# Optimization experiments

Measured on AMD Instinct MI355X. Metric: run time of the kernel, lower is better.

The kernel has to match this reference:

```python
import math
import jax, jax.numpy as jnp
import numpy as np

H_HEADS = 8
K_MAX = 64
MIN_WINDOW = 1.0
SHARPNESS = 5.0


def rmsnorm(x, w, eps=1e-6):
    x32 = x.astype(jnp.float32)
    var = jnp.mean(x32 * x32, axis=-1, keepdims=True)
    return (w * (x32 * jax.lax.rsqrt(var + eps))).astype(x.dtype)


def setup_inputs() -> dict:
    key = jax.random.key(0)
    ks = jax.random.split(key, 12)
    B, L, C = 1, 4096, 256
    H, K = H_HEADS, K_MAX
    s = 0.02
    return {
        "x": jax.random.normal(ks[0], (B, L, C), jnp.float32),
        "window_w": jax.random.normal(ks[1], (C, H), jnp.float32) * s,
        "window_b": jnp.zeros((H,), jnp.float32),
        "window_gamma": jnp.ones((H,), jnp.float32),
        "offset_w": jax.random.normal(ks[2], (C, H), jnp.float32) * s,
        "offset_b": jnp.zeros((H,), jnp.float32),
        "offset_gamma": jnp.ones((H,), jnp.float32),
        "kernel_w": jax.random.normal(ks[3], (C, H * K), jnp.float32) * s,
        "kernel_b": jnp.zeros((H * K,), jnp.float32),
        "kernel_gamma": jnp.ones((H * K,), jnp.float32),
        "v_w": jax.random.normal(ks[4], (C, C), jnp.float32) * (1.0 / math.sqrt(C)),
        "v_b": jnp.zeros((C,), jnp.float32),
        "out_w": jax.random.normal(ks[5], (C, C), jnp.float32) * s,
    }


def reference(x, window_w, window_b, window_gamma, offset_w, offset_b, offset_gamma,
              kernel_w, kernel_b, kernel_gamma, v_w, v_b, out_w):
    B, L, C = x.shape
    H, K = H_HEADS, K_MAX
    D = C // H
    max_window = min(int(math.sqrt(L)), K)
    half = max_window // 2
    max_offset = int(math.sqrt(L))
    N = 2 * half + 1  # num_offsets

    # per-position learned window sizes, center offsets, kernel weights
    window_raw = jax.nn.sigmoid(rmsnorm(x @ window_w + window_b, window_gamma))
    window_sizes = MIN_WINDOW + window_raw * (max_window - MIN_WINDOW)      # [B,L,H]
    center_offsets = jnp.tanh(rmsnorm(x @ offset_w + offset_b, offset_gamma)) * max_offset  # [B,L,H]
    kernel_weights = jax.nn.silu(rmsnorm(x @ kernel_w + kernel_b, kernel_gamma)).reshape(B, L, H, K)
    v = (x @ v_w + v_b).reshape(B, L, H, D)

    local = jnp.arange(-half, half + 1, dtype=x.dtype)                      # [N]
    positions = jnp.arange(L, dtype=x.dtype).reshape(1, L, 1, 1)
    neighbor = positions + center_offsets[..., None] + local.reshape(1, 1, 1, N)  # [B,L,H,N]
    valid = (neighbor >= 0) & (neighbor < L)
    nclamp = jnp.clip(neighbor, 0, L - 1)

    rel = jnp.abs(local).reshape(1, 1, 1, N) / (window_sizes[..., None] / 2 + 1e-6)
    window_mask = jax.nn.sigmoid(SHARPNESS * (1.0 - rel)) * valid.astype(x.dtype)

    # kernel interpolation by relative distance
    kidx = jnp.clip(rel, 0, 1) * (K - 1)
    i_fl = jnp.clip(kidx.astype(jnp.int32), 0, K - 2)                       # [B,L,H,N]
    i_ce = i_fl + 1
    w_ce = kidx - i_fl.astype(x.dtype)
    k_fl = jnp.take_along_axis(kernel_weights, i_fl, axis=-1)
    k_ce = jnp.take_along_axis(kernel_weights, i_ce, axis=-1)
    kernel_interp = k_fl * (1.0 - w_ce) + k_ce * w_ce

    attn = kernel_interp * window_mask
    attn = attn / (jnp.sum(attn, axis=-1, keepdims=True) + 1e-6)            # [B,L,H,N]

    # bilinear gather of values at fractional neighbor positions
    p_fl = jnp.clip(jnp.floor(nclamp).astype(jnp.int32), 0, L - 1)
    p_ce = jnp.clip(p_fl + 1, 0, L - 1)
    frac = nclamp - p_fl.astype(x.dtype)                                    # [B,L,H,N]

    v_bh = v.transpose(0, 2, 1, 3)                                          # [B,H,L,D]
    idx_f = p_fl.transpose(0, 2, 1, 3).reshape(B, H, L * N)
    idx_c = p_ce.transpose(0, 2, 1, 3).reshape(B, H, L * N)
    v_fl = jnp.take_along_axis(v_bh, idx_f[..., None], axis=2).reshape(B, H, L, N, D)
    v_ce = jnp.take_along_axis(v_bh, idx_c[..., None], axis=2).reshape(B, H, L, N, D)
    frac_bh = frac.transpose(0, 2, 1, 3)[..., None]                         # [B,H,L,N,1]
    v_nb = v_fl * (1.0 - frac_bh) + v_ce * frac_bh                          # [B,H,L,N,D]

    attn_bh = attn.transpose(0, 2, 1, 3)                                    # [B,H,L,N]
    out = jnp.einsum('bhln,bhlnd->bhld', attn_bh, v_nb)                     # [B,H,L,D]
    out = out.transpose(0, 2, 1, 3).reshape(B, L, C)
    return jax.nn.silu(out @ out_w)
```

## Files before the change

### kernel.cpp

```cpp
#include <hip/hip_runtime.h>
#include <math.h>

#define L_SEQ 4096
#define C_DIM 256
#define H_HEADS 8
#define K_MAX 64
#define D_HEAD 32
#define HALF_W 32
#define N_OFF 65
#define HK 512

__device__ __forceinline__ float sigmoidf_(float x) { return 1.0f / (1.0f + expf(-x)); }

__global__ void proj_gemm(const float* __restrict__ A, const float* __restrict__ kw_w,
                          const float* __restrict__ vw, const float* __restrict__ kb,
                          const float* __restrict__ vb,
                          float* __restrict__ kwbuf, float* __restrict__ vbuf) {
    __shared__ float As[16][132];
    __shared__ float Bs[16][68];

    const int tid = threadIdx.x;
    const int tx = tid & 15;
    const int ty = tid >> 4;
    const int l0 = blockIdx.y * 128;
    const int n0 = blockIdx.x * 64;

    const int ar0 = tid >> 2;
    const int ac0 = (tid & 3) * 4;
    const int ar1 = ar0 + 64;
    const int bk = tid >> 4;
    const int bn = (tid & 15) * 4;

    const float* Bsrc;
    int ldb, coff;
    if (n0 < 512) { Bsrc = kw_w; ldb = 512; coff = n0; }
    else          { Bsrc = vw;   ldb = 256; coff = n0 - 512; }

    float acc[8][4];
#pragma unroll
    for (int i = 0; i < 8; ++i)
#pragma unroll
        for (int jj = 0; jj < 4; ++jj) acc[i][jj] = 0.0f;

    float4 av0 = *(const float4*)&A[(l0 + ar0) * C_DIM + ac0];
    float4 av1 = *(const float4*)&A[(l0 + ar1) * C_DIM + ac0];
    float4 bv  = *(const float4*)&Bsrc[bk * ldb + coff + bn];

    for (int k0 = 0; k0 < C_DIM; k0 += 16) {
        __syncthreads();
        As[ac0 + 0][ar0] = av0.x;
        As[ac0 + 1][ar0] = av0.y;
        As[ac0 + 2][ar0] = av0.z;
        As[ac0 + 3][ar0] = av0.w;
        As[ac0 + 0][ar1] = av1.x;
        As[ac0 + 1][ar1] = av1.y;
        As[ac0 + 2][ar1] = av1.z;
        As[ac0 + 3][ar1] = av1.w;
        *(float4*)&Bs[bk][bn] = bv;
        __syncthreads();
        if (k0 + 16 < C_DIM) {
            av0 = *(const float4*)&A[(l0 + ar0) * C_DIM + (k0 + 16) + ac0];
            av1 = *(const float4*)&A[(l0 + ar1) * C_DIM + (k0 + 16) + ac0];
            bv  = *(const float4*)&Bsrc[(k0 + 16 + bk) * ldb + coff + bn];
        }
#pragma unroll
        for (int kk = 0; kk < 16; ++kk) {
            const float4 a4lo = *(const float4*)&As[kk][ty * 8];
            const float4 a4hi = *(const float4*)&As[kk][ty * 8 + 4];
            const float4 b4   = *(const float4*)&Bs[kk][tx * 4];
            const float ar[8] = {a4lo.x, a4lo.y, a4lo.z, a4lo.w,
                                 a4hi.x, a4hi.y, a4hi.z, a4hi.w};
            const float br[4] = {b4.x, b4.y, b4.z, b4.w};
#pragma unroll
            for (int i = 0; i < 8; ++i)
#pragma unroll
                for (int jj = 0; jj < 4; ++jj)
                    acc[i][jj] = fmaf(ar[i], br[jj], acc[i][jj]);
        }
    }

    const int g0 = n0 + tx * 4;
    float4 bz;
    float* dst;
    int stride, col;
    if (g0 < 512) { bz = *(const float4*)&kb[g0];       dst = kwbuf; stride = 512; col = g0; }
    else          { bz = *(const float4*)&vb[g0 - 512]; dst = vbuf;  stride = 256; col = g0 - 512; }
#pragma unroll
    for (int i = 0; i < 8; ++i) {
        const int row = l0 + ty * 8 + i;
        float4 o;
        o.x = acc[i][0] + bz.x;
        o.y = acc[i][1] + bz.y;
        o.z = acc[i][2] + bz.z;
        o.w = acc[i][3] + bz.w;
        *(float4*)&dst[row * stride + col] = o;
    }
}

__global__ void conv_fused(const float* __restrict__ x,
                           const float* __restrict__ ww, const float* __restrict__ wb,
                           const float* __restrict__ wg,
                           const float* __restrict__ ow, const float* __restrict__ ob,
                           const float* __restrict__ og,
                           const float* __restrict__ kg,
                           const float* __restrict__ kwraw, const float* __restrict__ v,
                           float* __restrict__ out) {
    const int l = blockIdx.x;
    const int tid = threadIdx.x;

    __shared__ float red[256];
    __shared__ float rs_s;
    __shared__ float kwrow[HK];
    __shared__ float wsz[H_HEADS], ofs[H_HEADS];
    __shared__ float4 tap[H_HEADS][N_OFF];
    __shared__ float inv_denom[H_HEADS];

    {
        const int j = tid;
        const float* row = kwraw + l * HK;
        const float z0 = row[j];
        const float z1 = row[j + 256];
        red[j] = z0 * z0 + z1 * z1;
        __syncthreads();
        for (int s = 128; s > 0; s >>= 1) {
            if (j < s) red[j] += red[j + s];
            __syncthreads();
        }
        if (j == 0) rs_s = rsqrtf(red[0] / (float)HK + 1e-6f);
        __syncthreads();
        const float rs = rs_s;
        const float n0v = kg[j] * z0 * rs;
        const float n1v = kg[j + 256] * z1 * rs;
        kwrow[j]       = n0v * sigmoidf_(n0v);
        kwrow[j + 256] = n1v * sigmoidf_(n1v);
    }

    if (tid < 64) {
        const int lane = tid;
        const float* xr = x + l * C_DIM;
        float accw[H_HEADS], acco[H_HEADS];
#pragma unroll
        for (int h = 0; h < H_HEADS; ++h) { accw[h] = 0.0f; acco[h] = 0.0f; }
#pragma unroll
        for (int i = 0; i < C_DIM / 64; ++i) {
            const int c = lane + i * 64;
            const float xv = xr[c];
            const float* wwc = ww + c * H_HEADS;
            const float* owc = ow + c * H_HEADS;
#pragma unroll
            for (int h = 0; h < H_HEADS; ++h) {
                accw[h] = fmaf(xv, wwc[h], accw[h]);
                acco[h] = fmaf(xv, owc[h], acco[h]);
            }
        }
#pragma unroll
        for (int off = 32; off > 0; off >>= 1) {
#pragma unroll
            for (int h = 0; h < H_HEADS; ++h) {
                accw[h] += __shfl_xor(accw[h], off);
                acco[h] += __shfl_xor(acco[h], off);
            }
        }
        if (lane < H_HEADS) {
            float zw[H_HEADS], zo[H_HEADS];
            float ssw = 0.0f, sso = 0.0f;
#pragma unroll
            for (int h = 0; h < H_HEADS; ++h) {
                zw[h] = accw[h] + wb[h];
                zo[h] = acco[h] + ob[h];
                ssw += zw[h] * zw[h];
                sso += zo[h] * zo[h];
            }
            const float rw = rsqrtf(ssw / (float)H_HEADS + 1e-6f);
            const float ro = rsqrtf(sso / (float)H_HEADS + 1e-6f);
            const float nw = wg[lane] * zw[lane] * rw;
            const float no = og[lane] * zo[lane] * ro;
            wsz[lane] = 1.0f + sigmoidf_(nw) * 63.0f;
            ofs[lane] = tanhf(no) * 64.0f;
        }
    }
    __syncthreads();

    for (int t = tid; t < H_HEADS * N_OFF; t += 256) {
        const int h = t / N_OFF;
        const int n = t - h * N_OFF;
        const float ws  = wsz[h];
        const float off = ofs[h];
        const float local = (float)(n - HALF_W);
        const float neighbor = (float)l + off + local;
        const bool valid = (neighbor >= 0.0f) && (neighbor < (float)L_SEQ);
        const float nc = fminf(fmaxf(neighbor, 0.0f), (float)(L_SEQ - 1));

        const float rel = fabsf(local) / (ws * 0.5f + 1e-6f);
        const float mask = sigmoidf_(5.0f * (1.0f - rel)) * (valid ? 1.0f : 0.0f);

        const float kidx = fminf(rel, 1.0f) * (float)(K_MAX - 1);
        int ifl = (int)kidx;
        ifl = min(ifl, K_MAX - 2);
        const float wce = kidx - (float)ifl;
        const float kf = kwrow[h * K_MAX + ifl];
        const float kc = kwrow[h * K_MAX + ifl + 1];
        const float attnv = (kf * (1.0f - wce) + kc * wce) * mask;

        int p = (int)floorf(nc);
        p = min(max(p, 0), L_SEQ - 1);
        const int pc = min(p + 1, L_SEQ - 1);
        const float fr = nc - (float)p;

        float4 tv;
        tv.x = attnv;
        tv.y = fr;
        tv.z = __int_as_float(p * C_DIM + h * D_HEAD);
        tv.w = __int_as_float(pc * C_DIM + h * D_HEAD);
        tap[h][n] = tv;
    }
    __syncthreads();

    if (tid < H_HEADS) {
        float s = 0.0f;
        for (int n = 0; n < N_OFF; ++n) s += tap[tid][n].x;
        inv_denom[tid] = 1.0f / (s + 1e-6f);
    }
    __syncthreads();

    const int h = tid >> 5;
    const int d = tid & 31;
    float acc = 0.0f;
#pragma unroll 5
    for (int n = 0; n < N_OFF; ++n) {
        const float4 t = tap[h][n];
        const int bf = __float_as_int(t.z);
        const int bc = __float_as_int(t.w);
        const float vf = v[bf + d];
        const float vc = v[bc + d];
        acc = fmaf(t.x, fmaf(t.y, vc - vf, vf), acc);
    }
    out[l * C_DIM + h * D_HEAD + d] = acc * inv_denom[h];
}

__global__ void out_gemm(const float* __restrict__ A, const float* __restrict__ W,
                         float* __restrict__ out) {
    __shared__ float As[16][36];
    __shared__ float Bs[16][68];

    const int tid = threadIdx.x;
    const int tx = tid & 15;
    const int ty = tid >> 4;
    const int l0 = blockIdx.y * 32;
    const int n0 = blockIdx.x * 64;

    const int bk = tid >> 4;
    const int bn = (tid & 15) * 4;
    const int am = (tid & 127) >> 2;
    const int ak = (tid & 3) * 4;
    const bool aload = tid < 128;

    float acc[2][4];
#pragma unroll
    for (int i = 0; i < 2; ++i)
#pragma unroll
        for (int jj = 0; jj < 4; ++jj) acc[i][jj] = 0.0f;

    float4 av, bv;
    if (aload) av = *(const float4*)&A[(l0 + am) * C_DIM + ak];
    bv = *(const float4*)&W[bk * C_DIM + n0 + bn];

    for (int k0 = 0; k0 < C_DIM; k0 += 16) {
        __syncthreads();
        if (aload) {
            As[ak + 0][am] = av.x;
            As[ak + 1][am] = av.y;
            As[ak + 2][am] = av.z;
            As[ak + 3][am] = av.w;
        }
        *(float4*)&Bs[bk][bn] = bv;
        __syncthreads();
        if (k0 + 16 < C_DIM) {
            if (aload) av = *(const float4*)&A[(l0 + am) * C_DIM + (k0 + 16) + ak];
            bv = *(const float4*)&W[(k0 + 16 + bk) * C_DIM + n0 + bn];
        }
#pragma unroll
        for (int kk = 0; kk < 16; ++kk) {
            const float a0 = As[kk][ty * 2 + 0];
            const float a1 = As[kk][ty * 2 + 1];
            const float4 b4 = *(const float4*)&Bs[kk][tx * 4];
            const float br[4] = {b4.x, b4.y, b4.z, b4.w};
#pragma unroll
            for (int jj = 0; jj < 4; ++jj) {
                acc[0][jj] = fmaf(a0, br[jj], acc[0][jj]);
                acc[1][jj] = fmaf(a1, br[jj], acc[1][jj]);
            }
        }
    }

    const int g0 = n0 + tx * 4;
#pragma unroll
    for (int i = 0; i < 2; ++i) {
        const int row = l0 + ty * 2 + i;
        float4 o;
        o.x = acc[i][0] * sigmoidf_(acc[i][0]);
        o.y = acc[i][1] * sigmoidf_(acc[i][1]);
        o.z = acc[i][2] * sigmoidf_(acc[i][2]);
        o.w = acc[i][3] * sigmoidf_(acc[i][3]);
        *(float4*)&out[row * C_DIM + g0] = o;
    }
}

extern "C" void kernel_launch(void* const* d_in, const int* in_sizes, int n_in,
                              void* d_out, int out_size, void* d_ws, size_t ws_size,
                              hipStream_t stream) {
    const float* x    = (const float*)d_in[0];
    const float* ww   = (const float*)d_in[1];
    const float* wb   = (const float*)d_in[2];
    const float* wg   = (const float*)d_in[3];
    const float* ow   = (const float*)d_in[4];
    const float* ob   = (const float*)d_in[5];
    const float* og   = (const float*)d_in[6];
    const float* kw_w = (const float*)d_in[7];
    const float* kb   = (const float*)d_in[8];
    const float* kg   = (const float*)d_in[9];
    const float* vw   = (const float*)d_in[10];
    const float* vb   = (const float*)d_in[11];
    const float* outw = (const float*)d_in[12];
    float* y = (float*)d_out;

    float* ws_f    = (float*)d_ws;
    float* kwbuf   = ws_f;
    float* vbuf    = kwbuf + L_SEQ * HK;
    float* convbuf = vbuf + L_SEQ * C_DIM;

    proj_gemm<<<dim3(12, L_SEQ / 128), 256, 0, stream>>>(x, kw_w, vw, kb, vb, kwbuf, vbuf);
    conv_fused<<<L_SEQ, 256, 0, stream>>>(x, ww, wb, wg, ow, ob, og, kg, kwbuf, vbuf, convbuf);
    out_gemm<<<dim3(C_DIM / 64, L_SEQ / 32), 256, 0, stream>>>(convbuf, outw, y);
}
```

Measured before the change: 154.2 us.

## Merge adjacent bilinear taps into single gathers; enlarge out_gemm tiles

The conv gather now precomputes merged weights per integer row, exploiting that tap n's ceil row equals tap n+1's floor row. That turns 130 loads per output into 66, with a runtime check that falls back to the original path when rows are not contiguous. Separately, out_gemm moves from 32x64 to 64x64 tiles with 4x4 per-thread outputs, giving more FMA reuse per shared-memory load but fewer blocks. The merge check adds a shared flag and an extra pass before the gather.

New measurement: 148.0 us. 1.04x faster.

```diff
diff --git a/kernel.cpp b/kernel.cpp
--- a/kernel.cpp
+++ b/kernel.cpp
@@ -113,7 +113,11 @@
     __shared__ float kwrow[HK];
     __shared__ float wsz[H_HEADS], ofs[H_HEADS];
     __shared__ float4 tap[H_HEADS][N_OFF];
+    __shared__ float2 warr[H_HEADS][N_OFF + 1];
     __shared__ float inv_denom[H_HEADS];
+    __shared__ int okflag;
+
+    if (tid == 0) okflag = 1;
 
     {
         const int j = tid;
@@ -216,6 +220,31 @@
     }
     __syncthreads();
 
+    for (int t = tid; t < H_HEADS * (N_OFF + 1); t += 256) {
+        const int h = t / (N_OFF + 1);
+        const int m = t - h * (N_OFF + 1);
+        float w, rowf;
+        if (m == 0) {
+            const float4 cur = tap[h][0];
+            w = cur.x * (1.0f - cur.y);
+            rowf = cur.z;
+        } else {
+            const float4 prev = tap[h][m - 1];
+            const float wc = prev.x * prev.y;
+            if (m < N_OFF) {
+                const float4 cur = tap[h][m];
+                w = cur.x * (1.0f - cur.y) + wc;
+                rowf = cur.z;
+                if (wc != 0.0f && __float_as_int(prev.w) != __float_as_int(cur.z))
+                    okflag = 0;
+            } else {
+                w = wc;
+                rowf = prev.w;
+            }
+        }
+        warr[h][m] = make_float2(w, rowf);
+    }
+
     if (tid < H_HEADS) {
         float s = 0.0f;
         for (int n = 0; n < N_OFF; ++n) s += tap[tid][n].x;
@@ -226,77 +255,81 @@
     const int h = tid >> 5;
     const int d = tid & 31;
     float acc = 0.0f;
+    if (okflag) {
+#pragma unroll 6
+        for (int m = 0; m < N_OFF + 1; ++m) {
+            const float2 t2 = warr[h][m];
+            acc = fmaf(t2.x, v[__float_as_int(t2.y) + d], acc);
+        }
+    } else {
 #pragma unroll 5
-    for (int n = 0; n < N_OFF; ++n) {
-        const float4 t = tap[h][n];
-        const int bf = __float_as_int(t.z);
-        const int bc = __float_as_int(t.w);
-        const float vf = v[bf + d];
-        const float vc = v[bc + d];
-        acc = fmaf(t.x, fmaf(t.y, vc - vf, vf), acc);
+        for (int n = 0; n < N_OFF; ++n) {
+            const float4 t4 = tap[h][n];
+            const int bf = __float_as_int(t4.z);
+            const int bc = __float_as_int(t4.w);
+            const float vf = v[bf + d];
+            const float vc = v[bc + d];
+            acc = fmaf(t4.x, fmaf(t4.y, vc - vf, vf), acc);
+        }
     }
     out[l * C_DIM + h * D_HEAD + d] = acc * inv_denom[h];
 }
 
 __global__ void out_gemm(const float* __restrict__ A, const float* __restrict__ W,
                          float* __restrict__ out) {
-    __shared__ float As[16][36];
+    __shared__ float As[16][68];
     __shared__ float Bs[16][68];
 
     const int tid = threadIdx.x;
     const int tx = tid & 15;
     const int ty = tid >> 4;
-    const int l0 = blockIdx.y * 32;
+    const int l0 = blockIdx.y * 64;
     const int n0 = blockIdx.x * 64;
 
+    const int am = tid >> 2;
+    const int ak = (tid & 3) * 4;
     const int bk = tid >> 4;
     const int bn = (tid & 15) * 4;
-    const int am = (tid & 127) >> 2;
-    const int ak = (tid & 3) * 4;
-    const bool aload = tid < 128;
-
-    float acc[2][4];
-#pragma unroll
-    for (int i = 0; i < 2; ++i)
+
+    float acc[4][4];
+#pragma unroll
+    for (int i = 0; i < 4; ++i)
 #pragma unroll
         for (int jj = 0; jj < 4; ++jj) acc[i][jj] = 0.0f;
 
-    float4 av, bv;
-    if (aload) av = *(const float4*)&A[(l0 + am) * C_DIM + ak];
-    bv = *(const float4*)&W[bk * C_DIM + n0 + bn];
+    float4 av = *(const float4*)&A[(l0 + am) * C_DIM + ak];
+    float4 bv = *(const float4*)&W[bk * C_DIM + n0 + bn];
 
     for (int k0 = 0; k0 < C_DIM; k0 += 16) {
         __syncthreads();
-        if (aload) {
-            As[ak + 0][am] = av.x;
-            As[ak + 1][am] = av.y;
-            As[ak + 2][am] = av.z;
-            As[ak + 3][am] = av.w;
-        }
+        As[ak + 0][am] = av.x;
+        As[ak + 1][am] = av.y;
+        As[ak + 2][am] = av.z;
+        As[ak + 3][am] = av.w;
         *(float4*)&Bs[bk][bn] = bv;
         __syncthreads();
         if (k0 + 16 < C_DIM) {
-            if (aload) av = *(const float4*)&A[(l0 + am) * C_DIM + (k0 + 16) + ak];
+            av = *(const float4*)&A[(l0 + am) * C_DIM + (k0 + 16) + ak];
             bv = *(const float4*)&W[(k0 + 16 + bk) * C_DIM + n0 + bn];
         }
 #pragma unroll
         for (int kk = 0; kk < 16; ++kk) {
-            const float a0 = As[kk][ty * 2 + 0];
-            const float a1 = As[kk][ty * 2 + 1];
+            const float4 a4 = *(const float4*)&As[kk][ty * 4];
             const float4 b4 = *(const float4*)&Bs[kk][tx * 4];
+            const float ar[4] = {a4.x, a4.y, a4.z, a4.w};
             const float br[4] = {b4.x, b4.y, b4.z, b4.w};
 #pragma unroll
-            for (int jj = 0; jj < 4; ++jj) {
-                acc[0][jj] = fmaf(a0, br[jj], acc[0][jj]);
-                acc[1][jj] = fmaf(a1, br[jj], acc[1][jj]);
-            }
+            for (int i = 0; i < 4; ++i)
+#pragma unroll
+                for (int jj = 0; jj < 4; ++jj)
+                    acc[i][jj] = fmaf(ar[i], br[jj], acc[i][jj]);
         }
     }
 
     const int g0 = n0 + tx * 4;
 #pragma unroll
-    for (int i = 0; i < 2; ++i) {
-        const int row = l0 + ty * 2 + i;
+    for (int i = 0; i < 4; ++i) {
+        const int row = l0 + ty * 4 + i;
         float4 o;
         o.x = acc[i][0] * sigmoidf_(acc[i][0]);
         o.y = acc[i][1] * sigmoidf_(acc[i][1]);
@@ -331,5 +364,5 @@
 
     proj_gemm<<<dim3(12, L_SEQ / 128), 256, 0, stream>>>(x, kw_w, vw, kb, vb, kwbuf, vbuf);
     conv_fused<<<L_SEQ, 256, 0, stream>>>(x, ww, wb, wg, ow, ob, og, kg, kwbuf, vbuf, convbuf);
-    out_gemm<<<dim3(C_DIM / 64, L_SEQ / 32), 256, 0, stream>>>(convbuf, outw, y);
+    out_gemm<<<dim3(C_DIM / 64, L_SEQ / 64), 256, 0, stream>>>(convbuf, outw, y);
 }
```
